# Performance work log

Measured on AMD Instinct MI355X. Metric: run time of the kernel, lower is better.

Reference implementation:

```python
import jax, jax.numpy as jnp
import numpy as np

N_NODES = 50000
N_EDGES = 800000
IN_F = 128
HEADS = 8
D_HEAD = 16  # out_features // num_heads = 128 // 8


def setup_inputs() -> dict:
    key = jax.random.key(0)
    k1, k2, k3, k4, k5 = jax.random.split(key, 5)
    x = jax.random.normal(k1, (N_NODES, IN_F), dtype=jnp.float32)
    edge_index = jax.random.randint(k2, (2, N_EDGES), 0, N_NODES, dtype=jnp.int64)
    # nn.Linear weight is [out, in]; xavier-ish scale
    W = jax.random.normal(k3, (HEADS * D_HEAD, IN_F), dtype=jnp.float32) * (1.0 / np.sqrt(IN_F))
    a_src = jax.random.normal(k4, (HEADS, D_HEAD), dtype=jnp.float32) * (1.0 / np.sqrt(D_HEAD))
    a_dst = jax.random.normal(k5, (HEADS, D_HEAD), dtype=jnp.float32) * (1.0 / np.sqrt(D_HEAD))
    return {"x": x, "edge_index": edge_index, "W": W, "a_src": a_src, "a_dst": a_dst}


def reference(x, edge_index, W, a_src, a_dst):
    N = x.shape[0]
    H, D = a_src.shape
    # h = W x, reshaped to [N, H, D]
    h = (x @ W.T).reshape(N, H, D)
    src, dst = edge_index[0], edge_index[1]
    # per-node attention logits, then gather per-edge (same math as gathering h first)
    s_src = jnp.einsum("nhd,hd->nh", h, a_src)  # [N, H]
    s_dst = jnp.einsum("nhd,hd->nh", h, a_dst)  # [N, H]
    attn = jax.nn.leaky_relu(s_src[src] + s_dst[dst], negative_slope=0.2)  # [E, H]
    # torch scatter_reduce amax onto a zeros tensor -> max is clamped at 0
    attn_max = jnp.maximum(jax.ops.segment_max(attn, dst, num_segments=N), 0.0)  # [N, H]
    e = jnp.exp(attn - attn_max[dst])  # [E, H]
    attn_sum = jax.ops.segment_sum(e, dst, num_segments=N)  # [N, H]
    alpha = e / (attn_sum[dst] + 1e-10)  # [E, H] (dropout is identity in eval)
    msg = h[src] * alpha[..., None]  # [E, H, D]
    out = jax.ops.segment_sum(msg, dst, num_segments=N)  # [N, H, D]
    return out.reshape(N, H * D)
```

## Files before the change

kernel.cpp:

```cpp
#include <hip/hip_runtime.h>
#include <hip/hip_bf16.h>

#define N_NODES 50000
#define N_EDGES 800000
#define HEADS 8
#define MAXDEG 64
#define NPB 4
#define NPART 8
#define PART_SZ 6250
#define CHUNK_EDGES 2048
#define NCHUNK ((N_EDGES + CHUNK_EDGES - 1) / CHUNK_EDGES)
#define NMFMA ((N_NODES + 127) / 128)
#define NFILLB (NCHUNK * NPART)

using frag_ab = __attribute__((ext_vector_type(8))) short;
using frag_cd = __attribute__((ext_vector_type(4))) float;

static __device__ __forceinline__ short f2bs(float v) {
    __hip_bfloat16 b = __float2bfloat16(v);
    return *(short*)&b;
}

__global__ __launch_bounds__(256) void k_wc(const float* __restrict__ W,
                                            const float* __restrict__ a_src,
                                            const float* __restrict__ a_dst,
                                            __hip_bfloat16* __restrict__ Wcb,
                                            int* __restrict__ cursor) {
    int tid = blockIdx.x * 256 + threadIdx.x;
    for (int i = tid; i < N_NODES; i += gridDim.x * 256) cursor[i] = 0;
    if (tid >= 144 * 128) return;
    int r = tid >> 7, k = tid & 127;
    float v;
    if (r < 128) {
        v = W[tid];
    } else {
        int hd = (r - 128) & 7;
        const float* av = (r < 136) ? a_src : a_dst;
        v = 0.f;
        #pragma unroll
        for (int d = 0; d < 16; ++d)
            v += av[hd * 16 + d] * W[(size_t)(hd * 16 + d) * 128 + k];
    }
    Wcb[tid] = __float2bfloat16(v);
}

__global__ __launch_bounds__(256) void k_fm(const float* __restrict__ x,
                                            const __hip_bfloat16* __restrict__ Wcb,
                                            __hip_bfloat16* __restrict__ hb,
                                            float* __restrict__ s_src,
                                            float* __restrict__ s_dst,
                                            const int* __restrict__ ei,
                                            int* __restrict__ cursor,
                                            int* __restrict__ csr_ell) {
    __shared__ short Ws[144][136];
    const int t = threadIdx.x;

    if (blockIdx.x >= NMFMA) {
        const int fb = blockIdx.x - NMFMA;
        const int part = fb & (NPART - 1);
        const int chunk = fb >> 3;
        const int lo = part * PART_SZ;
        const int e0 = chunk * CHUNK_EDGES;

        #pragma unroll
        for (int half = 0; half < 2; ++half) {
            int base = e0 + half * 1024 + t * 4;
            if (base >= N_EDGES) continue;
            int4 d4 = *(const int4*)(ei + N_EDGES + base);
            int4 s4 = *(const int4*)(ei + base);
            int dd[4] = { d4.x, d4.y, d4.z, d4.w };
            int ss[4] = { s4.x, s4.y, s4.z, s4.w };
            #pragma unroll
            for (int u = 0; u < 4; ++u) {
                unsigned rel = (unsigned)(dd[u] - lo);
                if (rel < PART_SZ) {
                    int pos = atomicAdd(&cursor[dd[u]], 1);
                    if (pos < MAXDEG) csr_ell[dd[u] * MAXDEG + pos] = ss[u];
                }
            }
        }
        return;
    }

    for (int i = t; i < 144 * 16; i += 256) {
        int r = i >> 4, c = (i & 15) << 3;
        frag_ab v = *(const frag_ab*)((const short*)Wcb + (size_t)r * 128 + c);
        *(frag_ab*)&Ws[r][c] = v;
    }
    __syncthreads();

    const int wave = t >> 6, lane = t & 63;
    const int rb0 = blockIdx.x * 128 + wave * 16;
    if (rb0 >= N_NODES) return;
    const int rb1 = rb0 + 64;
    const int m16 = lane & 15, kg = lane >> 4;
    const int arow0 = min(rb0 + m16, N_NODES - 1);
    const int arow1 = min(rb1 + m16, N_NODES - 1);
    const float* ab0 = x + (size_t)arow0 * 128 + kg * 8;
    const float* ab1 = x + (size_t)arow1 * 128 + kg * 8;

    frag_cd acc[2][9];
    #pragma unroll
    for (int r = 0; r < 2; ++r)
        #pragma unroll
        for (int j = 0; j < 9; ++j) acc[r][j] = (frag_cd){0.f, 0.f, 0.f, 0.f};

    #pragma unroll
    for (int ks = 0; ks < 4; ++ks) {
        float4 p0 = *(const float4*)(ab0 + ks * 32);
        float4 p1 = *(const float4*)(ab0 + ks * 32 + 4);
        float4 q0 = *(const float4*)(ab1 + ks * 32);
        float4 q1 = *(const float4*)(ab1 + ks * 32 + 4);
        frag_ab af0, af1;
        af0[0] = f2bs(p0.x); af0[1] = f2bs(p0.y); af0[2] = f2bs(p0.z); af0[3] = f2bs(p0.w);
        af0[4] = f2bs(p1.x); af0[5] = f2bs(p1.y); af0[6] = f2bs(p1.z); af0[7] = f2bs(p1.w);
        af1[0] = f2bs(q0.x); af1[1] = f2bs(q0.y); af1[2] = f2bs(q0.z); af1[3] = f2bs(q0.w);
        af1[4] = f2bs(q1.x); af1[5] = f2bs(q1.y); af1[6] = f2bs(q1.z); af1[7] = f2bs(q1.w);
        #pragma unroll
        for (int nt = 0; nt < 9; ++nt) {
            frag_ab bf = *(const frag_ab*)&Ws[nt * 16 + m16][ks * 32 + kg * 8];
            acc[0][nt] = __builtin_amdgcn_mfma_f32_16x16x32_bf16(af0, bf, acc[0][nt], 0, 0, 0);
            acc[1][nt] = __builtin_amdgcn_mfma_f32_16x16x32_bf16(af1, bf, acc[1][nt], 0, 0, 0);
        }
    }

    #pragma unroll
    for (int r = 0; r < 2; ++r) {
        int rbase = r ? rb1 : rb0;
        #pragma unroll
        for (int nt = 0; nt < 9; ++nt) {
            #pragma unroll
            for (int j = 0; j < 4; ++j) {
                int row = rbase + kg * 4 + j;
                if (row >= N_NODES) continue;
                int col = nt * 16 + m16;
                float v = acc[r][nt][j];
                if (col < 128)      hb[(size_t)row * 128 + col] = __float2bfloat16(v);
                else if (col < 136) s_src[row * 8 + (col - 128)] = v;
                else                s_dst[row * 8 + (col - 136)] = v;
            }
        }
    }
}

__global__ __launch_bounds__(256) void k_gather(const int* __restrict__ csr_ell,
                                                const int* __restrict__ cursor,
                                                const float* __restrict__ s_src,
                                                const float* __restrict__ s_dst,
                                                const __hip_bfloat16* __restrict__ hb,
                                                float* __restrict__ out) {
    __shared__ int   csr_l[NPB][MAXDEG];
    __shared__ float sa[NPB][MAXDEG][9];
    const int slot = threadIdx.x >> 6;
    const int lane = threadIdx.x & 63;
    const int n = blockIdx.x * NPB + slot;
    if (n >= N_NODES) return;
    const int hd8 = lane >> 3, l8 = lane & 7;
    const int deg = min(cursor[n], MAXDEG);
    const float sdst = s_dst[n * 8 + hd8];

    if (lane < deg) csr_l[slot][lane] = csr_ell[n * MAXDEG + lane];

    float m = 0.f;
    for (int j = l8; j < deg; j += 8) {
        float a = s_src[csr_l[slot][j] * 8 + hd8] + sdst;
        a = a > 0.f ? a : 0.2f * a;
        sa[slot][j][hd8] = a;
        m = fmaxf(m, a);
    }
    #pragma unroll
    for (int mask = 1; mask <= 4; mask <<= 1)
        m = fmaxf(m, __shfl_xor(m, mask));

    float s = 0.f;
    for (int j = l8; j < deg; j += 8) {
        float w = __expf(sa[slot][j][hd8] - m);
        sa[slot][j][hd8] = w;
        s += w;
    }
    #pragma unroll
    for (int mask = 1; mask <= 4; mask <<= 1)
        s += __shfl_xor(s, mask);
    float rcp = 1.0f / (s + 1e-10f);

    const int q = lane >> 4;
    const int fl = lane & 15;
    const int hd = fl >> 1;
    const float rcpq = __shfl(rcp, hd * 8);

    const unsigned short* hbs = (const unsigned short*)hb;
    float acc[8] = {0.f, 0.f, 0.f, 0.f, 0.f, 0.f, 0.f, 0.f};

    int j = 0;
    for (; j + 16 <= deg; j += 16) {
        int  jj0 = j + q,      jj1 = j + 4 + q,  jj2 = j + 8 + q,  jj3 = j + 12 + q;
        int  s0 = csr_l[slot][jj0], s1 = csr_l[slot][jj1];
        int  s2 = csr_l[slot][jj2], s3 = csr_l[slot][jj3];
        float w0 = sa[slot][jj0][hd], w1 = sa[slot][jj1][hd];
        float w2 = sa[slot][jj2][hd], w3 = sa[slot][jj3][hd];
        uint4 v0 = *(const uint4*)(hbs + (size_t)s0 * 128 + fl * 8);
        uint4 v1 = *(const uint4*)(hbs + (size_t)s1 * 128 + fl * 8);
        uint4 v2 = *(const uint4*)(hbs + (size_t)s2 * 128 + fl * 8);
        uint4 v3 = *(const uint4*)(hbs + (size_t)s3 * 128 + fl * 8);
        #define ACC8(vv, ww) \
            acc[0] += (ww) * __uint_as_float((vv).x << 16); \
            acc[1] += (ww) * __uint_as_float((vv).x & 0xffff0000u); \
            acc[2] += (ww) * __uint_as_float((vv).y << 16); \
            acc[3] += (ww) * __uint_as_float((vv).y & 0xffff0000u); \
            acc[4] += (ww) * __uint_as_float((vv).z << 16); \
            acc[5] += (ww) * __uint_as_float((vv).z & 0xffff0000u); \
            acc[6] += (ww) * __uint_as_float((vv).w << 16); \
            acc[7] += (ww) * __uint_as_float((vv).w & 0xffff0000u);
        ACC8(v0, w0) ACC8(v1, w1) ACC8(v2, w2) ACC8(v3, w3)
    }
    for (; j + 4 <= deg; j += 4) {
        int jj = j + q;
        int src = csr_l[slot][jj];
        float w = sa[slot][jj][hd];
        uint4 v = *(const uint4*)(hbs + (size_t)src * 128 + fl * 8);
        ACC8(v, w)
    }
    if (j < deg) {
        int jj = j + q;
        if (jj < deg) {
            int src = csr_l[slot][jj];
            float w = sa[slot][jj][hd];
            uint4 v = *(const uint4*)(hbs + (size_t)src * 128 + fl * 8);
            ACC8(v, w)
        }
    }
    #undef ACC8

    #pragma unroll
    for (int k = 0; k < 8; ++k) {
        acc[k] += __shfl_xor(acc[k], 16);
        acc[k] += __shfl_xor(acc[k], 32);
    }
    if (q == 0) {
        float4 o0 = { acc[0] * rcpq, acc[1] * rcpq, acc[2] * rcpq, acc[3] * rcpq };
        float4 o1 = { acc[4] * rcpq, acc[5] * rcpq, acc[6] * rcpq, acc[7] * rcpq };
        *(float4*)(out + (size_t)n * 128 + fl * 8)     = o0;
        *(float4*)(out + (size_t)n * 128 + fl * 8 + 4) = o1;
    }
}

extern "C" void kernel_launch(void* const* d_in, const int* in_sizes, int n_in,
                              void* d_out, int out_size, void* d_ws, size_t ws_size,
                              hipStream_t stream) {
    const float* x     = (const float*)d_in[0];
    const int*   ei    = (const int*)d_in[1];
    const float* W     = (const float*)d_in[2];
    const float* a_src = (const float*)d_in[3];
    const float* a_dst = (const float*)d_in[4];
    float* out = (float*)d_out;

    char* ws = (char*)d_ws;
    __hip_bfloat16* hb      = (__hip_bfloat16*)(ws);
    __hip_bfloat16* Wcb     = (__hip_bfloat16*)(ws + 12800000);
    float*          s_src   = (float*)(ws + 12840000);
    float*          s_dst   = (float*)(ws + 14440000);
    int*            cursor  = (int*)  (ws + 16040000);
    int*            csr_ell = (int*)  (ws + 16240000);

    k_wc    <<<(144 * 128 + 255) / 256, 256, 0, stream>>>(W, a_src, a_dst, Wcb, cursor);
    k_fm    <<<NMFMA + NFILLB, 256, 0, stream>>>(x, Wcb, hb, s_src, s_dst, ei, cursor, csr_ell);
    k_gather<<<(N_NODES + NPB - 1) / NPB, 256, 0, stream>>>(csr_ell, cursor, s_src, s_dst, hb, out);
}
```

Baseline: 91.19 us.

## Assign CSR fill partitions by XCC id via per-partition work queues

Fill blocks now read their hardware XCC id and take the destination partition matching it. Chunks come from a per-partition atomic queue, and blocks steal from other partitions once their own queue is empty. Each XCC then mostly performs atomics and scattered writes to one contiguous node range, so cursor and csr lines should stay in that XCC's L2 rather than bouncing between dies. The cost is extra global atomics per block, a block-wide sync, and a dependence on an undocumented hardware register mapping.

Result: slower. 107.8 us (+18.3%).

```diff
diff --git a/kernel.cpp b/kernel.cpp
--- a/kernel.cpp
+++ b/kernel.cpp
@@ -25,9 +25,9 @@
                                             const float* __restrict__ a_src,
                                             const float* __restrict__ a_dst,
                                             __hip_bfloat16* __restrict__ Wcb,
-                                            int* __restrict__ cursor) {
+                                            int* __restrict__ cursor_q) {
     int tid = blockIdx.x * 256 + threadIdx.x;
-    for (int i = tid; i < N_NODES; i += gridDim.x * 256) cursor[i] = 0;
+    for (int i = tid; i < N_NODES + NPART; i += gridDim.x * 256) cursor_q[i] = 0;
     if (tid >= 144 * 128) return;
     int r = tid >> 7, k = tid & 127;
     float v;
@@ -51,17 +51,35 @@
                                             float* __restrict__ s_dst,
                                             const int* __restrict__ ei,
                                             int* __restrict__ cursor,
+                                            int* __restrict__ qctr,
                                             int* __restrict__ csr_ell) {
     __shared__ short Ws[144][136];
+    __shared__ int sh_chunk, sh_part;
     const int t = threadIdx.x;
 
     if (blockIdx.x >= NMFMA) {
-        const int fb = blockIdx.x - NMFMA;
-        const int part = fb & (NPART - 1);
-        const int chunk = fb >> 3;
+        if (t == 0) {
+            unsigned xcc;
+            asm volatile("s_getreg_b32 %0, hwreg(HW_REG_XCC_ID)" : "=s"(xcc));
+            int part = (int)(xcc & (NPART - 1));
+            int chunk = atomicAdd(&qctr[part], 1);
+            if (chunk >= NCHUNK) {
+                chunk = -1;
+                for (int pp = 0; pp < NPART; ++pp) {
+                    int c2 = atomicAdd(&qctr[pp], 1);
+                    if (c2 < NCHUNK) { chunk = c2; part = pp; break; }
+                }
+            }
+            sh_chunk = chunk;
+            sh_part = part;
+        }
+        __syncthreads();
+        const int chunk = sh_chunk;
+        const int part = sh_part;
+        if (chunk < 0) return;
+
         const int lo = part * PART_SZ;
         const int e0 = chunk * CHUNK_EDGES;
-
         #pragma unroll
         for (int half = 0; half < 2; ++half) {
             int base = e0 + half * 1024 + t * 4;
@@ -260,9 +278,10 @@
     float*          s_src   = (float*)(ws + 12840000);
     float*          s_dst   = (float*)(ws + 14440000);
     int*            cursor  = (int*)  (ws + 16040000);
-    int*            csr_ell = (int*)  (ws + 16240000);
+    int*            qctr    = (int*)  (ws + 16240000);
+    int*            csr_ell = (int*)  (ws + 16240064);
 
     k_wc    <<<(144 * 128 + 255) / 256, 256, 0, stream>>>(W, a_src, a_dst, Wcb, cursor);
-    k_fm    <<<NMFMA + NFILLB, 256, 0, stream>>>(x, Wcb, hb, s_src, s_dst, ei, cursor, csr_ell);
+    k_fm    <<<NMFMA + NFILLB, 256, 0, stream>>>(x, Wcb, hb, s_src, s_dst, ei, cursor, qctr, csr_ell);
     k_gather<<<(N_NODES + NPB - 1) / NPB, 256, 0, stream>>>(csr_ell, cursor, s_src, s_dst, hb, out);
 }
```

## Build ELL adjacency via two-pass bucket sort with shared-memory atomics

Applied to the files above, without the earlier changes.

Global atomics per edge on a per-node cursor are replaced with a two-phase scheme. First, edge blocks make a local histogram of destination buckets and reserve space with one global atomic per bucket, then scatter (src,dst) pairs into bucket buffers. A new kernel then builds the ELL rows per bucket using shared-memory cursors. This removes the 8x redundant partitioned scan of the edge list and the contended global atomics, at the cost of an extra kernel launch, an 8-byte intermediate write and read per edge, and a fixed bucket capacity that could overflow.

After: 84.15 us. 7.7% less time.

```diff
diff --git a/kernel.cpp b/kernel.cpp
--- a/kernel.cpp
+++ b/kernel.cpp
@@ -6,12 +6,11 @@
 #define HEADS 8
 #define MAXDEG 64
 #define NPB 4
-#define NPART 8
-#define PART_SZ 6250
-#define CHUNK_EDGES 2048
-#define NCHUNK ((N_EDGES + CHUNK_EDGES - 1) / CHUNK_EDGES)
 #define NMFMA ((N_NODES + 127) / 128)
-#define NFILLB (NCHUNK * NPART)
+#define NBINB 391
+#define NBUCK 128
+#define BUCK_NODES 391
+#define BUCK_CAP 12288
 
 using frag_ab = __attribute__((ext_vector_type(8))) short;
 using frag_cd = __attribute__((ext_vector_type(4))) float;
@@ -25,9 +24,9 @@
                                             const float* __restrict__ a_src,
                                             const float* __restrict__ a_dst,
                                             __hip_bfloat16* __restrict__ Wcb,
-                                            int* __restrict__ cursor) {
+                                            int* __restrict__ gcount) {
     int tid = blockIdx.x * 256 + threadIdx.x;
-    for (int i = tid; i < N_NODES; i += gridDim.x * 256) cursor[i] = 0;
+    if (tid < NBUCK) gcount[tid] = 0;
     if (tid >= 144 * 128) return;
     int r = tid >> 7, k = tid & 127;
     float v;
@@ -50,33 +49,50 @@
                                             float* __restrict__ s_src,
                                             float* __restrict__ s_dst,
                                             const int* __restrict__ ei,
-                                            int* __restrict__ cursor,
-                                            int* __restrict__ csr_ell) {
+                                            int* __restrict__ gcount,
+                                            int2* __restrict__ bbuf) {
     __shared__ short Ws[144][136];
     const int t = threadIdx.x;
 
     if (blockIdx.x >= NMFMA) {
+        __shared__ int hist[NBUCK];
+        __shared__ int basei[NBUCK];
         const int fb = blockIdx.x - NMFMA;
-        const int part = fb & (NPART - 1);
-        const int chunk = fb >> 3;
-        const int lo = part * PART_SZ;
-        const int e0 = chunk * CHUNK_EDGES;
-
-        #pragma unroll
-        for (int half = 0; half < 2; ++half) {
-            int base = e0 + half * 1024 + t * 4;
-            if (base >= N_EDGES) continue;
-            int4 d4 = *(const int4*)(ei + N_EDGES + base);
-            int4 s4 = *(const int4*)(ei + base);
-            int dd[4] = { d4.x, d4.y, d4.z, d4.w };
-            int ss[4] = { s4.x, s4.y, s4.z, s4.w };
+        for (int i = t; i < NBUCK; i += 256) hist[i] = 0;
+        __syncthreads();
+
+        const int e0 = fb * 2048 + t * 8;
+        const bool active = (e0 + 8 <= N_EDGES);
+        int srcs[8], dsts[8], bks[8];
+        if (active) {
+            int4 s0 = *(const int4*)(ei + e0);
+            int4 s1 = *(const int4*)(ei + e0 + 4);
+            int4 d0 = *(const int4*)(ei + N_EDGES + e0);
+            int4 d1 = *(const int4*)(ei + N_EDGES + e0 + 4);
+            srcs[0] = s0.x; srcs[1] = s0.y; srcs[2] = s0.z; srcs[3] = s0.w;
+            srcs[4] = s1.x; srcs[5] = s1.y; srcs[6] = s1.z; srcs[7] = s1.w;
+            dsts[0] = d0.x; dsts[1] = d0.y; dsts[2] = d0.z; dsts[3] = d0.w;
+            dsts[4] = d1.x; dsts[5] = d1.y; dsts[6] = d1.z; dsts[7] = d1.w;
             #pragma unroll
-            for (int u = 0; u < 4; ++u) {
-                unsigned rel = (unsigned)(dd[u] - lo);
-                if (rel < PART_SZ) {
-                    int pos = atomicAdd(&cursor[dd[u]], 1);
-                    if (pos < MAXDEG) csr_ell[dd[u] * MAXDEG + pos] = ss[u];
-                }
+            for (int u = 0; u < 8; ++u) {
+                bks[u] = dsts[u] / BUCK_NODES;
+                atomicAdd(&hist[bks[u]], 1);
+            }
+        }
+        __syncthreads();
+        if (t < NBUCK) {
+            int h = hist[t];
+            basei[t] = h ? atomicAdd(&gcount[t], h) : 0;
+            hist[t] = 0;
+        }
+        __syncthreads();
+        if (active) {
+            #pragma unroll
+            for (int u = 0; u < 8; ++u) {
+                int off = atomicAdd(&hist[bks[u]], 1);
+                int pos = basei[bks[u]] + off;
+                if (pos < BUCK_CAP)
+                    bbuf[bks[u] * BUCK_CAP + pos] = make_int2(srcs[u], dsts[u]);
             }
         }
         return;
@@ -141,6 +157,28 @@
             }
         }
     }
+}
+
+__global__ __launch_bounds__(256) void k_ell(const int2* __restrict__ bbuf,
+                                             const int* __restrict__ gcount,
+                                             int* __restrict__ cursor,
+                                             int* __restrict__ csr_ell) {
+    __shared__ int cur[BUCK_NODES];
+    const int b = blockIdx.x;
+    const int t = threadIdx.x;
+    const int lo = b * BUCK_NODES;
+    const int hi = min(lo + BUCK_NODES, N_NODES);
+    const int ncur = hi - lo;
+    for (int i = t; i < ncur; i += 256) cur[i] = 0;
+    __syncthreads();
+    const int cnt = min(gcount[b], BUCK_CAP);
+    for (int i = t; i < cnt; i += 256) {
+        int2 e = bbuf[(size_t)b * BUCK_CAP + i];
+        int pos = atomicAdd(&cur[e.y - lo], 1);
+        if (pos < MAXDEG) csr_ell[e.y * MAXDEG + pos] = e.x;
+    }
+    __syncthreads();
+    for (int i = t; i < ncur; i += 256) cursor[lo + i] = cur[i];
 }
 
 __global__ __launch_bounds__(256) void k_gather(const int* __restrict__ csr_ell,
@@ -260,9 +298,12 @@
     float*          s_src   = (float*)(ws + 12840000);
     float*          s_dst   = (float*)(ws + 14440000);
     int*            cursor  = (int*)  (ws + 16040000);
-    int*            csr_ell = (int*)  (ws + 16240000);
-
-    k_wc    <<<(144 * 128 + 255) / 256, 256, 0, stream>>>(W, a_src, a_dst, Wcb, cursor);
-    k_fm    <<<NMFMA + NFILLB, 256, 0, stream>>>(x, Wcb, hb, s_src, s_dst, ei, cursor, csr_ell);
+    int*            gcount  = (int*)  (ws + 16240000);
+    int*            csr_ell = (int*)  (ws + 16241024);
+    int2*           bbuf    = (int2*) (ws + 29041024);
+
+    k_wc    <<<(144 * 128 + 255) / 256, 256, 0, stream>>>(W, a_src, a_dst, Wcb, gcount);
+    k_fm    <<<NMFMA + NBINB, 256, 0, stream>>>(x, Wcb, hb, s_src, s_dst, ei, gcount, bbuf);
+    k_ell   <<<NBUCK, 256, 0, stream>>>(bbuf, gcount, cursor, csr_ell);
     k_gather<<<(N_NODES + NPB - 1) / NPB, 256, 0, stream>>>(csr_ell, cursor, s_src, s_dst, hb, out);
 }
```
